# Optimization experiments

Hardware: AMD Instinct MI355X
Metric: run time of the kernel (lower is better)

Reference implementation:

```python
import jax, jax.numpy as jnp
import numpy as np

D = 384            # lattice_size
PIX = 1.0          # pixel_size (Angstrom)
SIGMA = 1.5        # gaussian width
QUALITY = 3.0
K = int(np.ceil(QUALITY * SIGMA / PIX) * 2 + 1)  # n_pix_cutoff = 11


def setup_inputs() -> dict:
    key = jax.random.key(0)
    k1, k2, k3, k4 = jax.random.split(key, 4)
    # atom coords spread over the box (box spans ~[-192, 192] Angstrom)
    crd = jax.random.normal(k1, (64, 8192, 3), jnp.float32) * 60.0
    # per-image pose: orthonormalize to proper rotation-like matrices
    rot, _ = jnp.linalg.qr(jax.random.normal(k2, (64, 3, 3), jnp.float32))
    rot_init, _ = jnp.linalg.qr(jax.random.normal(k3, (3, 3), jnp.float32))
    trans_init = jax.random.normal(k4, (3,), jnp.float32) * 2.0
    return {"crd": crd, "rot": rot, "rot_init": rot_init, "trans_init": trans_init}


def _splat(crd):
    # crd: [B, N, 3]; project onto x-y plane and splat gaussians into [B, D, D]
    c = crd[..., :2] / PIX + D // 2                      # pixel-space coords [B,N,2]
    center = jnp.round(c).astype(jnp.int32)              # nearest pixel [B,N,2]
    offs = jnp.arange(K, dtype=jnp.int32) - K // 2       # [K]
    ix = center[..., 0, None] + offs                     # [B,N,K]
    iy = center[..., 1, None] + offs                     # [B,N,K]
    px = (ix.astype(crd.dtype) - D // 2) * PIX           # physical pixel coords
    py = (iy.astype(crd.dtype) - D // 2) * PIX
    inv2s2 = 1.0 / (2.0 * SIGMA * SIGMA)
    mx = ((ix >= 0) & (ix < D)).astype(crd.dtype)
    my = ((iy >= 0) & (iy < D)).astype(crd.dtype)
    gx = jnp.exp(-(px - crd[..., 0, None]) ** 2 * inv2s2) * mx   # [B,N,K]
    gy = jnp.exp(-(py - crd[..., 1, None]) ** 2 * inv2s2) * my   # [B,N,K]
    vals = gy[..., :, None] * gx[..., None, :]                   # [B,N,K,K]
    idx = (jnp.clip(iy, 0, D - 1)[..., :, None] * D
           + jnp.clip(ix, 0, D - 1)[..., None, :])               # [B,N,K,K]

    def splat_one(v, i):
        return jnp.zeros(D * D, v.dtype).at[i.reshape(-1)].add(v.reshape(-1))

    img = jax.vmap(splat_one)(vals, idx)
    return img.reshape(crd.shape[0], D, D)


def reference(crd, rot, rot_init, trans_init):
    # pose the atoms
    crd = crd @ rot_init + trans_init[None, None, :]
    crd = jnp.einsum('bnj,bkj->bnk', crd, rot)           # crd @ rot^T
    # gaussian pixel splatting (gather/cutoff/scatter)
    y_real = _splat(crd)                                  # [B,D,D]
    # centered 2D FFT
    f = jnp.fft.fftshift(
        jnp.fft.fftn(jnp.fft.fftshift(y_real, axes=(-2, -1)), axes=(-2, -1)),
        axes=(-2, -1))
    y = f.real - f.imag                                   # hartley domain
    return y, y_real
```

## Files before the change

kernel.cpp:

```cpp
#include <hip/hip_runtime.h>

#define DD 384
#define NB 64
#define NATOM 8192
#define RB 394
#define CB 51
#define NBKT (RB * CB)
#define OFFSTRIDE (NBKT + 4)
#define NCH 4
#define CHSZ 5120

typedef short short8 __attribute__((ext_vector_type(8)));
typedef float f32x4 __attribute__((ext_vector_type(4)));
typedef unsigned u32x4 __attribute__((ext_vector_type(4)));

__device__ inline unsigned bf1(float a) {
    unsigned u = __float_as_uint(a);
    return (u + 0x7FFFu + ((u >> 16) & 1u)) >> 16;
}
__device__ inline unsigned bfpack(float a, float b) {
    return bf1(a) | (bf1(b) << 16);
}

__device__ inline float2 pose_one(const float* __restrict__ crd,
                                  const float* __restrict__ rot,
                                  const float* __restrict__ rot_init,
                                  const float* __restrict__ trans, int idx) {
    int b = idx >> 13;
    const float* p = crd + (long)idx * 3;
    float x0 = p[0], y0 = p[1], z0 = p[2];
    float q0 = x0 * rot_init[0] + y0 * rot_init[3] + z0 * rot_init[6] + trans[0];
    float q1 = x0 * rot_init[1] + y0 * rot_init[4] + z0 * rot_init[7] + trans[1];
    float q2 = x0 * rot_init[2] + y0 * rot_init[5] + z0 * rot_init[8] + trans[2];
    const float* R = rot + b * 9;
    float2 o;
    o.x = q0 * R[0] + q1 * R[1] + q2 * R[2];
    o.y = q0 * R[3] + q1 * R[4] + q2 * R[5];
    return o;
}

__global__ void count_atoms(const float* __restrict__ crd,
                            const float* __restrict__ rot,
                            const float* __restrict__ rot_init,
                            const float* __restrict__ trans,
                            int* __restrict__ counts,
                            float2* __restrict__ posed) {
    int idx = blockIdx.x * 256 + threadIdx.x;
    float2 v = pose_one(crd, rot, rot_init, trans, idx);
    posed[idx] = v;
    int icx = (int)rintf(v.x + 192.0f);
    int icy = (int)rintf(v.y + 192.0f);
    if (icx < -5 || icx > 388 || icy < -5 || icy > 388) return;
    int bi = (icy + 5) * CB + ((icx + 16) >> 3);
    atomicAdd(&counts[(idx >> 13) * NBKT + bi], 1);
}

__global__ __launch_bounds__(1024) void scan_a(int* __restrict__ counts,
                                               int* __restrict__ offs,
                                               int* __restrict__ chunktot) {
    int bc = blockIdx.x;
    int b = bc >> 2, ch = bc & 3;
    int base = ch * CHSZ;
    int t = threadIdx.x, lane = t & 63, wid = t >> 6;
    int* cnt = counts + b * NBKT;
    int* off = offs + b * OFFSTRIDE;
    __shared__ int wsum[16];
    __shared__ int carrySm;
    if (t == 0) carrySm = 0;
    __syncthreads();
    for (int tile = 0; tile < 5; ++tile) {
        int k = base + tile * 1024 + t;
        int v = (k < NBKT) ? cnt[k] : 0;
        int incl = v;
#pragma unroll
        for (int d = 1; d < 64; d <<= 1) {
            int u = __shfl_up(incl, d);
            if (lane >= d) incl += u;
        }
        if (lane == 63) wsum[wid] = incl;
        __syncthreads();
        if (wid == 0) {
            int s = (lane < 16) ? wsum[lane] : 0;
            int si = s;
#pragma unroll
            for (int d = 1; d < 16; d <<= 1) {
                int u = __shfl_up(si, d);
                if (lane >= d) si += u;
            }
            if (lane < 16) wsum[lane] = si - s;
        }
        __syncthreads();
        int excl = incl - v + wsum[wid] + carrySm;
        if (k < NBKT) {
            off[k] = excl;
            cnt[k] = 0;
        }
        __syncthreads();
        if (t == 1023) carrySm = excl + v;
        __syncthreads();
    }
    if (t == 0) chunktot[bc] = carrySm;
}

__global__ __launch_bounds__(1024) void scan_b(int* __restrict__ offs,
                                               const int* __restrict__ chunktot) {
    int bc = blockIdx.x;
    int b = bc >> 2, ch = bc & 3;
    const int* ct = chunktot + b * NCH;
    int* off = offs + b * OFFSTRIDE;
    int t = threadIdx.x;
    if (ch == 0) {
        if (t == 0) off[NBKT] = ct[0] + ct[1] + ct[2] + ct[3];
        return;
    }
    int basev = 0;
    for (int i = 0; i < ch; i++) basev += ct[i];
    int k0 = ch * CHSZ;
    for (int tile = 0; tile < 5; ++tile) {
        int k = k0 + tile * 1024 + t;
        if (k < NBKT) off[k] += basev;
    }
}

__global__ void scatter_atoms(const float2* __restrict__ posed,
                              int* __restrict__ cursors,
                              const int* __restrict__ offs,
                              float2* __restrict__ sorted) {
    int idx = blockIdx.x * 256 + threadIdx.x;
    float2 v = posed[idx];
    int icx = (int)rintf(v.x + 192.0f);
    int icy = (int)rintf(v.y + 192.0f);
    if (icx < -5 || icx > 388 || icy < -5 || icy > 388) return;
    int b = idx >> 13;
    int bi = (icy + 5) * CB + ((icx + 16) >> 3);
    int pos = offs[b * OFFSTRIDE + bi] + atomicAdd(&cursors[b * NBKT + bi], 1);
    sorted[(long)b * NATOM + pos] = v;
}

#define LCAP 512
#define LSZ  544

__global__ __launch_bounds__(256) void splat_mfma(const float2* __restrict__ sorted,
                                                  const int* __restrict__ offs,
                                                  float* __restrict__ img,
                                                  unsigned short* __restrict__ img_bf) {
    __shared__ __align__(16) float2 list[4][LSZ];
    int b = blockIdx.z;
    int wv = __builtin_amdgcn_readfirstlane((int)(threadIdx.x >> 6));
    int lane = threadIdx.x & 63;
    int tx = blockIdx.x * 4 + wv;
    int ty = blockIdx.y;
    int c0 = tx * 16, r0 = ty * 16;

    const int* off = offs + b * OFFSTRIDE;
    const float2* srt = sorted + (long)b * NATOM;

    int cb_lo = (c0 + 11) >> 3;
    int cb_end = ((c0 + 36) >> 3) + 1;

    int cur = 0, iend = 0;
    if (lane < 26) {
        int rb = r0 + lane;
        cur = off[rb * CB + cb_lo];
        iend = off[rb * CB + cb_end];
    }

    f32x4 acc = {0.f, 0.f, 0.f, 0.f};
    int m = lane & 15;
    float rowf = (float)(r0 + m);
    float colf = (float)(c0 + m);
    float py = rowf - 192.0f, px = colf - 192.0f;
    int g8 = (lane >> 4) << 3;
    const float kneg = -0.32059868f;
    float2* wl = list[wv];

    for (int round = 0; round < 24; ++round) {
        int len = (lane < 26) ? (iend - cur) : 0;
        int incl = len;
#pragma unroll
        for (int d = 1; d < 64; d <<= 1) {
            int t = __shfl_up(incl, d);
            if (lane >= d) incl += t;
        }
        int excl = incl - len;
        int totrem = __builtin_amdgcn_readfirstlane(__shfl(incl, 63));
        if (totrem == 0) break;
        int total = min(totrem, LCAP);
        int cnt = min(len, max(0, LCAP - excl));
        for (int j = 0; j < cnt; j++) wl[excl + j] = srt[cur + j];
        cur += cnt;
        int padn = (32 - (total & 31)) & 31;
        if (lane < padn) wl[total + lane] = (float2){3.0e5f, 3.0e5f};
        asm volatile("s_waitcnt lgkmcnt(0)" ::: "memory");
        __builtin_amdgcn_sched_barrier(0);

        int nch = (total + 31) >> 5;
        for (int ch = 0; ch < nch; ch++) {
            const f32x4* qp = (const f32x4*)&wl[ch * 32 + g8];
            u32x4 au, bu;
#pragma unroll
            for (int p = 0; p < 4; p++) {
                f32x4 q = qp[p];
                float d0 = py - q[1], d1 = py - q[3];
                float cy0 = rintf(q[1] + 192.0f), cy1 = rintf(q[3] + 192.0f);
                float e0 = (fabsf(rowf - cy0) <= 5.0f) ? exp2f(d0 * d0 * kneg) : 0.0f;
                float e1 = (fabsf(rowf - cy1) <= 5.0f) ? exp2f(d1 * d1 * kneg) : 0.0f;
                au[p] = bfpack(e0, e1);
                float f0 = px - q[0], f1 = px - q[2];
                float cx0 = rintf(q[0] + 192.0f), cx1 = rintf(q[2] + 192.0f);
                float g0 = (fabsf(colf - cx0) <= 5.0f) ? exp2f(f0 * f0 * kneg) : 0.0f;
                float g1 = (fabsf(colf - cx1) <= 5.0f) ? exp2f(f1 * f1 * kneg) : 0.0f;
                bu[p] = bfpack(g0, g1);
            }
            short8 af = __builtin_bit_cast(short8, au);
            short8 bf = __builtin_bit_cast(short8, bu);
            acc = __builtin_amdgcn_mfma_f32_16x16x32_bf16(af, bf, acc, 0, 0, 0);
        }
        if (totrem <= LCAP) break;
    }

    int col = c0 + m;
    int rbase = r0 + (lane >> 4) * 4;
#pragma unroll
    for (int r = 0; r < 4; r++) {
        long o = ((long)b * DD + rbase + r) * DD + col;
        img[o] = acc[r];
        img_bf[o] = (unsigned short)bf1(acc[r]);
    }
}

__global__ void gen_w(unsigned short* __restrict__ Bt1,
                      unsigned short* __restrict__ Bt2) {
    int idx = blockIdx.x * 256 + threadIdx.x;
    if (idx >= DD * DD) return;
    int i = idx / DD, j = idx % DD;
    int t = (i - 192) * (j - 192);
    int r = t % DD;
    if (r < 0) r += DD;
    float th = (float)r * (6.28318530717958647692f / (float)DD);
    float s = sinf(th), c = cosf(th);
    Bt1[i * DD + j] = (unsigned short)bf1(c + s);
    Bt1[(DD + i) * DD + j] = (unsigned short)bf1(s);
    Bt2[i * 768 + j] = (unsigned short)bf1(c + s);
    Bt2[i * 768 + 384 + j] = (unsigned short)bf1(-2.0f * s);
}

template <bool CBF16, bool BFOLD>
__global__ __launch_bounds__(256) void gemm_mfma(const unsigned short* __restrict__ Ag,
                                                 const unsigned short* __restrict__ Bg,
                                                 long sB,
                                                 void* __restrict__ Cg, long sC,
                                                 int K, int ldc, int nx, int bpi) {
    __shared__ uint4 lds4[2048];

    int cpx = gridDim.x >> 3;
    int wg = blockIdx.x;
    int lin = (wg & 7) * cpx + (wg >> 3);
    int bz = lin / bpi;
    int rr = lin - bz * bpi;
    int m0 = (rr / nx) * 128, n0 = (rr % nx) * 128;
    int tid = threadIdx.x;
    int lane = tid & 63, w = tid >> 6;
    int wm = w >> 1, wn = w & 1;

    f32x4 acc[4][4];
#pragma unroll
    for (int i = 0; i < 4; i++)
#pragma unroll
        for (int j = 0; j < 4; j++) acc[i][j] = (f32x4){0.f, 0.f, 0.f, 0.f};

    const unsigned short* Bh = Bg + (long)bz * sB;

    int lsw = lane ^ (((lane >> 4) & 3) << 1);

    for (int k0 = 0; k0 < K; k0 += 64) {
        __syncthreads();
#pragma unroll
        for (int cc = 0; cc < 4; cc++) {
            int c = tid + cc * 256;
            int m = c >> 3, kc = (c & 7) << 3;
            int li = ((m >> 4) * 2 + (kc >> 5)) * 64 +
                     ((m & 15) | (((kc >> 3) & 3) << 4));
            li ^= ((kc >> 3) & 3) << 1;
            lds4[li] = *(const uint4*)(Ag + (long)(m0 + m) * K + k0 + kc);
            uint4 wv;
            if (BFOLD) {
                int kk = k0 + kc;
                long boff = (kk >= 384)
                                ? ((long)(384 + n0 + m) * 384 + (kk - 384))
                                : ((long)(n0 + m) * 384 + kk);
                wv = *(const uint4*)(Bh + boff);
            } else {
                wv = *(const uint4*)(Bh + (long)(n0 + m) * K + k0 + kc);
            }
            lds4[1024 + li] = wv;
        }
        __syncthreads();
#pragma unroll
        for (int ki = 0; ki < 2; ki++) {
            short8 a[4], bfr[4];
#pragma unroll
            for (int i = 0; i < 4; i++)
                a[i] = *(const short8*)&lds4[((wm * 4 + i) * 2 + ki) * 64 + lsw];
#pragma unroll
            for (int j = 0; j < 4; j++)
                bfr[j] = *(const short8*)&lds4[1024 + ((wn * 4 + j) * 2 + ki) * 64 + lsw];
#pragma unroll
            for (int i = 0; i < 4; i++)
#pragma unroll
                for (int j = 0; j < 4; j++)
                    acc[i][j] = __builtin_amdgcn_mfma_f32_16x16x32_bf16(
                        a[i], bfr[j], acc[i][j], 0, 0, 0);
        }
    }

    int quad = lane >> 4, col0 = lane & 15;
#pragma unroll
    for (int i = 0; i < 4; i++)
#pragma unroll
        for (int j = 0; j < 4; j++)
#pragma unroll
            for (int r = 0; r < 4; r++) {
                int row = m0 + (wm * 4 + i) * 16 + quad * 4 + r;
                int cc2 = n0 + (wn * 4 + j) * 16 + col0;
                if (CBF16)
                    ((unsigned short*)Cg + (long)bz * sC)[(long)row * ldc + cc2] =
                        (unsigned short)bf1(acc[i][j][r]);
                else
                    ((float*)Cg + (long)bz * sC)[(long)row * ldc + cc2] = acc[i][j][r];
            }
}

extern "C" void kernel_launch(void* const* d_in, const int* in_sizes, int n_in,
                              void* d_out, int out_size, void* d_ws, size_t ws_size,
                              hipStream_t stream) {
    const float* crd      = (const float*)d_in[0];
    const float* rot      = (const float*)d_in[1];
    const float* rot_init = (const float*)d_in[2];
    const float* trans    = (const float*)d_in[3];

    float* out   = (float*)d_out;
    float* y     = out;
    float* yreal = out + (size_t)NB * DD * DD;
    unsigned short* Ybf = (unsigned short*)y;

    char* ws = (char*)d_ws;
    unsigned short* Bt1 = (unsigned short*)ws;
    unsigned short* Bt2 = (unsigned short*)(ws + 589824);
    char* Zb = ws + 1179648;
    unsigned short* Z = (unsigned short*)Zb;
    int*    counts  = (int*)Zb;
    int*    offs    = (int*)(Zb + 5144064);
    float2* sorted  = (float2*)(Zb + 10289152);
    float2* posed   = (float2*)(Zb + 14483456);
    int*    chunktot= (int*)(Zb + 18677760);

    hipMemsetAsync(counts, 0, (size_t)NB * NBKT * 4, stream);

    count_atoms<<<(NB * NATOM) / 256, 256, 0, stream>>>(crd, rot, rot_init, trans,
                                                        counts, posed);
    scan_a<<<NB * NCH, 1024, 0, stream>>>(counts, offs, chunktot);
    scan_b<<<NB * NCH, 1024, 0, stream>>>(offs, chunktot);
    scatter_atoms<<<(NB * NATOM) / 256, 256, 0, stream>>>(posed, counts, offs, sorted);
    splat_mfma<<<dim3(6, 24, NB), 256, 0, stream>>>(sorted, offs, yreal, Ybf);

    gen_w<<<(DD * DD + 255) / 256, 256, 0, stream>>>(Bt1, Bt2);

    gemm_mfma<true, false><<<1152, 256, 0, stream>>>(
        Bt1, Ybf, (long)DD * DD, (void*)Z, (long)768 * DD, DD, DD, 3, 18);

    gemm_mfma<false, true><<<576, 256, 0, stream>>>(
        Bt2, Z, (long)768 * DD, (void*)y, (long)DD * DD, 768, DD, 3, 9);
}
```

Measured before the change: 254.4 us.

## Enlarge splat tile per wavefront to 32x32 with four MFMA accumulators

Each wavefront now covers a 32x32 pixel tile instead of 16x16, using four 16x16 MFMA accumulators that share the atom list loaded into LDS. Because the neighbourhood halo is amortised over a bigger tile, fewer atoms are loaded redundantly per output pixel, and the grid shrinks by four. The costs are more registers, a larger LDS list, fewer blocks (less parallelism), and relatively more gaussian evaluations for atoms that touch only part of the tile.

```diff
diff --git a/kernel.cpp b/kernel.cpp
--- a/kernel.cpp
+++ b/kernel.cpp
@@ -137,8 +137,8 @@
     sorted[(long)b * NATOM + pos] = v;
 }
 
-#define LCAP 512
-#define LSZ  544
+#define LCAP 768
+#define LSZ  800
 
 __global__ __launch_bounds__(256) void splat_mfma(const float2* __restrict__ sorted,
                                                   const int* __restrict__ offs,
@@ -150,32 +150,34 @@
     int lane = threadIdx.x & 63;
     int tx = blockIdx.x * 4 + wv;
     int ty = blockIdx.y;
-    int c0 = tx * 16, r0 = ty * 16;
+    int c0 = tx * 32, r0 = ty * 32;
 
     const int* off = offs + b * OFFSTRIDE;
     const float2* srt = sorted + (long)b * NATOM;
 
     int cb_lo = (c0 + 11) >> 3;
-    int cb_end = ((c0 + 36) >> 3) + 1;
+    int cb_end = ((c0 + 52) >> 3) + 1;
 
     int cur = 0, iend = 0;
-    if (lane < 26) {
+    if (lane < 42) {
         int rb = r0 + lane;
         cur = off[rb * CB + cb_lo];
         iend = off[rb * CB + cb_end];
     }
 
-    f32x4 acc = {0.f, 0.f, 0.f, 0.f};
+    f32x4 acc00 = {0.f, 0.f, 0.f, 0.f}, acc01 = {0.f, 0.f, 0.f, 0.f};
+    f32x4 acc10 = {0.f, 0.f, 0.f, 0.f}, acc11 = {0.f, 0.f, 0.f, 0.f};
     int m = lane & 15;
-    float rowf = (float)(r0 + m);
-    float colf = (float)(c0 + m);
-    float py = rowf - 192.0f, px = colf - 192.0f;
+    float rowf0 = (float)(r0 + m), rowf1 = rowf0 + 16.0f;
+    float colf0 = (float)(c0 + m), colf1 = colf0 + 16.0f;
+    float py0 = rowf0 - 192.0f, py1 = py0 + 16.0f;
+    float px0 = colf0 - 192.0f, px1 = px0 + 16.0f;
     int g8 = (lane >> 4) << 3;
     const float kneg = -0.32059868f;
     float2* wl = list[wv];
 
     for (int round = 0; round < 24; ++round) {
-        int len = (lane < 26) ? (iend - cur) : 0;
+        int len = (lane < 42) ? (iend - cur) : 0;
         int incl = len;
 #pragma unroll
         for (int d = 1; d < 64; d <<= 1) {
@@ -197,35 +199,52 @@
         int nch = (total + 31) >> 5;
         for (int ch = 0; ch < nch; ch++) {
             const f32x4* qp = (const f32x4*)&wl[ch * 32 + g8];
-            u32x4 au, bu;
+            u32x4 au0, au1, bu0, bu1;
 #pragma unroll
             for (int p = 0; p < 4; p++) {
                 f32x4 q = qp[p];
-                float d0 = py - q[1], d1 = py - q[3];
                 float cy0 = rintf(q[1] + 192.0f), cy1 = rintf(q[3] + 192.0f);
-                float e0 = (fabsf(rowf - cy0) <= 5.0f) ? exp2f(d0 * d0 * kneg) : 0.0f;
-                float e1 = (fabsf(rowf - cy1) <= 5.0f) ? exp2f(d1 * d1 * kneg) : 0.0f;
-                au[p] = bfpack(e0, e1);
-                float f0 = px - q[0], f1 = px - q[2];
                 float cx0 = rintf(q[0] + 192.0f), cx1 = rintf(q[2] + 192.0f);
-                float g0 = (fabsf(colf - cx0) <= 5.0f) ? exp2f(f0 * f0 * kneg) : 0.0f;
-                float g1 = (fabsf(colf - cx1) <= 5.0f) ? exp2f(f1 * f1 * kneg) : 0.0f;
-                bu[p] = bfpack(g0, g1);
+                float d0 = py0 - q[1], d1 = py0 - q[3];
+                float e00 = (fabsf(rowf0 - cy0) <= 5.0f) ? exp2f(d0 * d0 * kneg) : 0.0f;
+                float e01 = (fabsf(rowf0 - cy1) <= 5.0f) ? exp2f(d1 * d1 * kneg) : 0.0f;
+                au0[p] = bfpack(e00, e01);
+                float d2 = py1 - q[1], d3 = py1 - q[3];
+                float e10 = (fabsf(rowf1 - cy0) <= 5.0f) ? exp2f(d2 * d2 * kneg) : 0.0f;
+                float e11 = (fabsf(rowf1 - cy1) <= 5.0f) ? exp2f(d3 * d3 * kneg) : 0.0f;
+                au1[p] = bfpack(e10, e11);
+                float f0 = px0 - q[0], f1 = px0 - q[2];
+                float g00 = (fabsf(colf0 - cx0) <= 5.0f) ? exp2f(f0 * f0 * kneg) : 0.0f;
+                float g01 = (fabsf(colf0 - cx1) <= 5.0f) ? exp2f(f1 * f1 * kneg) : 0.0f;
+                bu0[p] = bfpack(g00, g01);
+                float f2 = px1 - q[0], f3 = px1 - q[2];
+                float g10 = (fabsf(colf1 - cx0) <= 5.0f) ? exp2f(f2 * f2 * kneg) : 0.0f;
+                float g11 = (fabsf(colf1 - cx1) <= 5.0f) ? exp2f(f3 * f3 * kneg) : 0.0f;
+                bu1[p] = bfpack(g10, g11);
             }
-            short8 af = __builtin_bit_cast(short8, au);
-            short8 bf = __builtin_bit_cast(short8, bu);
-            acc = __builtin_amdgcn_mfma_f32_16x16x32_bf16(af, bf, acc, 0, 0, 0);
+            short8 a0 = __builtin_bit_cast(short8, au0);
+            short8 a1 = __builtin_bit_cast(short8, au1);
+            short8 b0 = __builtin_bit_cast(short8, bu0);
+            short8 b1 = __builtin_bit_cast(short8, bu1);
+            acc00 = __builtin_amdgcn_mfma_f32_16x16x32_bf16(a0, b0, acc00, 0, 0, 0);
+            acc01 = __builtin_amdgcn_mfma_f32_16x16x32_bf16(a0, b1, acc01, 0, 0, 0);
+            acc10 = __builtin_amdgcn_mfma_f32_16x16x32_bf16(a1, b0, acc10, 0, 0, 0);
+            acc11 = __builtin_amdgcn_mfma_f32_16x16x32_bf16(a1, b1, acc11, 0, 0, 0);
         }
         if (totrem <= LCAP) break;
     }
 
-    int col = c0 + m;
-    int rbase = r0 + (lane >> 4) * 4;
+    int q4 = (lane >> 4) * 4;
 #pragma unroll
     for (int r = 0; r < 4; r++) {
-        long o = ((long)b * DD + rbase + r) * DD + col;
-        img[o] = acc[r];
-        img_bf[o] = (unsigned short)bf1(acc[r]);
+        long o00 = ((long)b * DD + r0 + q4 + r) * DD + c0 + m;
+        long o01 = ((long)b * DD + r0 + q4 + r) * DD + c0 + 16 + m;
+        long o10 = ((long)b * DD + r0 + 16 + q4 + r) * DD + c0 + m;
+        long o11 = ((long)b * DD + r0 + 16 + q4 + r) * DD + c0 + 16 + m;
+        img[o00] = acc00[r];  img_bf[o00] = (unsigned short)bf1(acc00[r]);
+        img[o01] = acc01[r];  img_bf[o01] = (unsigned short)bf1(acc01[r]);
+        img[o10] = acc10[r];  img_bf[o10] = (unsigned short)bf1(acc10[r]);
+        img[o11] = acc11[r];  img_bf[o11] = (unsigned short)bf1(acc11[r]);
     }
 }
 
@@ -362,7 +381,7 @@
     scan_a<<<NB * NCH, 1024, 0, stream>>>(counts, offs, chunktot);
     scan_b<<<NB * NCH, 1024, 0, stream>>>(offs, chunktot);
     scatter_atoms<<<(NB * NATOM) / 256, 256, 0, stream>>>(posed, counts, offs, sorted);
-    splat_mfma<<<dim3(6, 24, NB), 256, 0, stream>>>(sorted, offs, yreal, Ybf);
+    splat_mfma<<<dim3(3, 12, NB), 256, 0, stream>>>(sorted, offs, yreal, Ybf);
 
     gen_w<<<(DD * DD + 255) / 256, 256, 0, stream>>>(Bt1, Bt2);
 
```

Result: slower. 277.2 us (+9.0%).
